# Optimization experiments

Hardware: AMD Instinct MI355X
Metric: run time of the kernel (lower is better)

Reference implementation:

```python
import jax, jax.numpy as jnp
import numpy as np

CAPACITY_FACTOR = 1.25  # config.capacity_factor


def setup_inputs() -> dict:
    key = jax.random.key(0)
    ks = jax.random.split(key, 5)
    B, S, D, F, E = 8, 2048, 768, 3072, 8
    return {
        "x": jax.random.normal(ks[0], (B, S, D), jnp.float32),
        "switch_w": jax.random.normal(ks[1], (D, E), jnp.float32) * 0.02,
        "switch_b": jnp.zeros((E,), jnp.float32),
        "w1": jax.random.normal(ks[2], (E, D, F), jnp.float32) * 0.02,
        "b1": jnp.zeros((E, F), jnp.float32),
        "w2": jax.random.normal(ks[3], (E, F, D), jnp.float32) * 0.02,
        "b2": jnp.zeros((E, D), jnp.float32),
    }


def reference(x, switch_w, switch_b, w1, b1, w2, b2):
    B, S, D = x.shape
    E = w1.shape[0]
    xf = x.reshape(-1, D)                      # [N, D] tokens
    N = xf.shape[0]
    capacity = int(CAPACITY_FACTOR * N / E)

    # top-1 switch routing
    probs = jax.nn.softmax(xf @ switch_w + switch_b, axis=-1)   # [N, E]
    prob_max = jnp.max(probs, axis=-1)                          # [N]
    routes = jnp.argmax(probs, axis=-1)                         # [N] int

    # priority drop: within each expert keep the `capacity` tokens with
    # highest gate prob. Rank tokens within their expert by descending prob.
    sort_idx = jnp.lexsort((-prob_max, routes))                 # [N]
    counts = jnp.bincount(routes, length=E)
    starts = jnp.concatenate([jnp.zeros((1,), counts.dtype), jnp.cumsum(counts)[:-1]])
    rank_sorted = jnp.arange(N) - starts[routes[sort_idx]]
    rank = jnp.zeros((N,), jnp.int32).at[sort_idx].set(rank_sorted.astype(jnp.int32))
    keep = rank < capacity

    # dispatch kept tokens into [E, capacity, D]; overflow goes to slot E
    dest_e = jnp.where(keep, routes, E)
    dest_c = jnp.where(keep, rank, 0)
    buf = jnp.zeros((E + 1, capacity, D), xf.dtype).at[dest_e, dest_c].set(xf)

    # per-expert FFN (grouped GEMM), GELU is exact (erf) as in nn.GELU()
    h = jax.nn.gelu(jnp.einsum('ecd,edf->ecf', buf[:E], w1) + b1[:, None, :],
                    approximate=False)
    o = jnp.einsum('ecf,efd->ecd', h, w2) + b2[:, None, :]      # [E, cap, D]

    # combine: kept tokens get expert output, dropped tokens pass through x
    y_exp = o[routes, dest_c]                                    # [N, D]
    y = jnp.where(keep[:, None], y_exp, xf)
    out = y * prob_max[:, None]                                  # is_scale_prob
    return out.reshape(B, S, D)
```

## Files before the change

kernel.cpp:

```cpp
#include <hip/hip_runtime.h>
#include <cstdint>
#include <cstddef>

#define E_ 8
#define D_ 768
#define F_ 3072
#define N_ 16384
#define CAP_ 2560
#define NCHUNK_ (N_ / 256)

typedef __attribute__((ext_vector_type(8))) short bf16x8;
typedef __attribute__((ext_vector_type(4))) float f32x4;

__device__ __forceinline__ unsigned short f2bf(float f) {
  unsigned u = __float_as_uint(f);
  u += 0x7fffu + ((u >> 16) & 1u);
  return (unsigned short)(u >> 16);
}

__device__ __forceinline__ void gload16(const void* g, void* l) {
  __builtin_amdgcn_global_load_lds(
      (const __attribute__((address_space(1))) void*)g,
      (__attribute__((address_space(3))) void*)l, 16, 0, 0);
}

__global__ void tcast_kernel(const float* __restrict__ src, unsigned short* __restrict__ dst,
                             int R, int C) {
  __shared__ float tile[64][65];
  int e = blockIdx.z;
  const float* s = src + (size_t)e * R * C;
  unsigned short* d = dst + (size_t)e * R * C;
  int c0 = blockIdx.x * 64, r0 = blockIdx.y * 64;
  int tx = threadIdx.x, ty = threadIdx.y;
  #pragma unroll
  for (int rr = ty; rr < 64; rr += 8) {
    tile[rr][tx]      = s[(size_t)(r0 + rr) * C + c0 + tx];
    tile[rr][tx + 32] = s[(size_t)(r0 + rr) * C + c0 + tx + 32];
  }
  __syncthreads();
  #pragma unroll
  for (int cc = ty; cc < 64; cc += 8) {
    ushort2 o;
    o.x = f2bf(tile[2 * tx][cc]);
    o.y = f2bf(tile[2 * tx + 1][cc]);
    *(ushort2*)&d[(size_t)(c0 + cc) * R + r0 + 2 * tx] = o;
  }
}

__global__ __launch_bounds__(256) void router_kernel(
    const float* __restrict__ x, const float* __restrict__ sw, const float* __restrict__ sb,
    int* __restrict__ route, float* __restrict__ prob,
    unsigned short* __restrict__ xb) {
  __shared__ float wl[E_ * D_];
  int tid = threadIdx.x;
  #pragma unroll
  for (int ee = 0; ee < E_; ++ee)
    for (int dd = tid; dd < D_; dd += 256)
      wl[ee * D_ + dd] = sw[dd * E_ + ee];
  __syncthreads();
  int wave = tid >> 6, lane = tid & 63;
  int tbase = blockIdx.x * 16 + wave * 4;
  #pragma unroll
  for (int tt = 0; tt < 4; ++tt) {
    int t = tbase + tt;
    const float* xp = x + (size_t)t * D_;
    unsigned short* xbp = xb + (size_t)t * D_;
    float acc[E_];
    #pragma unroll
    for (int e = 0; e < E_; ++e) acc[e] = 0.f;
    #pragma unroll
    for (int r = 0; r < D_ / 64; ++r) {
      int dd = r * 64 + lane;
      float xv = xp[dd];
      xbp[dd] = f2bf(xv);
      #pragma unroll
      for (int e = 0; e < E_; ++e) acc[e] += xv * wl[e * D_ + dd];
    }
    #pragma unroll
    for (int e = 0; e < E_; ++e) {
      #pragma unroll
      for (int o = 32; o > 0; o >>= 1) acc[e] += __shfl_xor(acc[e], o);
    }
    if (lane == 0) {
      float mx = -1e30f; int arg = 0;
      #pragma unroll
      for (int e = 0; e < E_; ++e) {
        float l = acc[e] + sb[e];
        acc[e] = l;
        if (l > mx) { mx = l; arg = e; }
      }
      float s = 0.f;
      #pragma unroll
      for (int e = 0; e < E_; ++e) s += expf(acc[e] - mx);
      route[t] = arg;
      prob[t] = 1.f / s;
    }
  }
}

__global__ void hist_kernel(const int* __restrict__ route, int* __restrict__ chunk_hist) {
  __shared__ int h[E_];
  int tid = threadIdx.x;
  if (tid < E_) h[tid] = 0;
  __syncthreads();
  atomicAdd(&h[route[blockIdx.x * 256 + tid]], 1);
  __syncthreads();
  if (tid < E_) chunk_hist[blockIdx.x * E_ + tid] = h[tid];
}

__global__ void scan_kernel(const int* __restrict__ chunk_hist, int* __restrict__ chunk_off,
                            int* __restrict__ counts) {
  __shared__ int h[NCHUNK_ * E_];
  int tid = threadIdx.x;
  h[tid] = chunk_hist[tid];
  __syncthreads();
  if (tid < E_) {
    int run = 0;
    for (int c = 0; c < NCHUNK_; ++c) {
      chunk_off[c * E_ + tid] = run;
      run += h[c * E_ + tid];
    }
    counts[tid] = run;
  }
}

__global__ void assign_kernel(const int* __restrict__ route, const float* __restrict__ prob,
                              const int* __restrict__ counts, const int* __restrict__ chunk_off,
                              int* __restrict__ tok_list, int* __restrict__ slot) {
  __shared__ int rt[256];
  int tid = threadIdx.x;
  int i = blockIdx.x * 256 + tid;
  int e = route[i];
  rt[tid] = e;
  __syncthreads();
  int r = 0;
  for (int j = 0; j < tid; ++j) r += (rt[j] == e) ? 1 : 0;
  int c = counts[e];
  int s; bool keep;
  if (c <= CAP_) {
    s = chunk_off[blockIdx.x * E_ + e] + r;
    keep = true;
  } else {
    float p = prob[i];
    int rr = 0;
    for (int j = 0; j < N_; ++j) {
      if (route[j] == e) {
        float pj = prob[j];
        rr += (pj > p || (pj == p && j < i)) ? 1 : 0;
      }
    }
    s = rr; keep = (rr < CAP_);
  }
  if (keep) tok_list[e * CAP_ + s] = i;
  slot[i] = keep ? s : -1;
}

__global__ __launch_bounds__(256) void gemm1_kernel(
    const unsigned short* __restrict__ xb, const unsigned short* __restrict__ w1t,
    const float* __restrict__ b1, const int* __restrict__ tok_list,
    const int* __restrict__ counts, unsigned short* __restrict__ hb) {
  int e = blockIdx.z;
  int Me = counts[e] < CAP_ ? counts[e] : CAP_;
  int m0 = blockIdx.x * 128;
  if (m0 >= Me) return;
  int n0 = blockIdx.y * 128;
  __shared__ unsigned short At[128 * 32];
  __shared__ unsigned short Bt[128 * 32];
  int tid = threadIdx.x, lane = tid & 63, wave = tid >> 6;
  int rA0 = (wave * 2 + 0) * 16 + (lane >> 2);
  int rA1 = (wave * 2 + 1) * 16 + (lane >> 2);
  int cb = (lane & 3) * 16;
  int mr0 = m0 + rA0; if (mr0 > Me - 1) mr0 = Me - 1;
  int mr1 = m0 + rA1; if (mr1 > Me - 1) mr1 = Me - 1;
  int tok0 = tok_list[e * CAP_ + mr0];
  int tok1 = tok_list[e * CAP_ + mr1];
  const char* gA0 = (const char*)(xb + (size_t)tok0 * D_) + cb;
  const char* gA1 = (const char*)(xb + (size_t)tok1 * D_) + cb;
  const char* gB0 = (const char*)(w1t + ((size_t)e * F_ + n0 + rA0) * D_) + cb;
  const char* gB1 = (const char*)(w1t + ((size_t)e * F_ + n0 + rA1) * D_) + cb;
  unsigned short* lA0 = At + (wave * 2 + 0) * 512;
  unsigned short* lA1 = At + (wave * 2 + 1) * 512;
  unsigned short* lB0 = Bt + (wave * 2 + 0) * 512;
  unsigned short* lB1 = Bt + (wave * 2 + 1) * 512;
  f32x4 acc[4][4] = {};
  int wm = (wave >> 1) * 64, wn = (wave & 1) * 64;
  int fr = lane & 15, fk = (lane >> 4) * 8;
  for (int k0 = 0; k0 < D_; k0 += 32) {
    __syncthreads();
    gload16(gA0 + (size_t)2 * k0, lA0);
    gload16(gA1 + (size_t)2 * k0, lA1);
    gload16(gB0 + (size_t)2 * k0, lB0);
    gload16(gB1 + (size_t)2 * k0, lB1);
    __syncthreads();
    bf16x8 a[4], b[4];
    #pragma unroll
    for (int i = 0; i < 4; ++i)
      a[i] = *(const bf16x8*)(At + (wm + i * 16 + fr) * 32 + fk);
    #pragma unroll
    for (int j = 0; j < 4; ++j)
      b[j] = *(const bf16x8*)(Bt + (wn + j * 16 + fr) * 32 + fk);
    #pragma unroll
    for (int i = 0; i < 4; ++i)
      #pragma unroll
      for (int j = 0; j < 4; ++j)
        acc[i][j] = __builtin_amdgcn_mfma_f32_16x16x32_bf16(a[i], b[j], acc[i][j], 0, 0, 0);
  }
  int q4 = (lane >> 4) * 4;
  #pragma unroll
  for (int i = 0; i < 4; ++i) {
    #pragma unroll
    for (int j = 0; j < 4; ++j) {
      int col = n0 + wn + j * 16 + (lane & 15);
      float bias = b1[e * F_ + col];
      #pragma unroll
      for (int r = 0; r < 4; ++r) {
        int row = m0 + wm + i * 16 + q4 + r;
        if (row < Me) {
          float v = acc[i][j][r] + bias;
          v = 0.5f * v * (1.f + erff(v * 0.70710678118654752f));
          hb[((size_t)e * CAP_ + row) * F_ + col] = f2bf(v);
        }
      }
    }
  }
}

__global__ __launch_bounds__(256) void gemm2_kernel(
    const unsigned short* __restrict__ hb, const unsigned short* __restrict__ w2t,
    const float* __restrict__ b2, const int* __restrict__ tok_list,
    const int* __restrict__ counts, const float* __restrict__ prob,
    float* __restrict__ out) {
  int e = blockIdx.z;
  int Me = counts[e] < CAP_ ? counts[e] : CAP_;
  int m0 = blockIdx.x * 128;
  if (m0 >= Me) return;
  int n0 = blockIdx.y * 128;
  __shared__ unsigned short At[128 * 32];
  __shared__ unsigned short Bt[128 * 32];
  int tid = threadIdx.x, lane = tid & 63, wave = tid >> 6;
  int rA0 = (wave * 2 + 0) * 16 + (lane >> 2);
  int rA1 = (wave * 2 + 1) * 16 + (lane >> 2);
  int cb = (lane & 3) * 16;
  const char* gA0 = (const char*)(hb + ((size_t)e * CAP_ + m0 + rA0) * F_) + cb;
  const char* gA1 = (const char*)(hb + ((size_t)e * CAP_ + m0 + rA1) * F_) + cb;
  const char* gB0 = (const char*)(w2t + ((size_t)e * D_ + n0 + rA0) * F_) + cb;
  const char* gB1 = (const char*)(w2t + ((size_t)e * D_ + n0 + rA1) * F_) + cb;
  unsigned short* lA0 = At + (wave * 2 + 0) * 512;
  unsigned short* lA1 = At + (wave * 2 + 1) * 512;
  unsigned short* lB0 = Bt + (wave * 2 + 0) * 512;
  unsigned short* lB1 = Bt + (wave * 2 + 1) * 512;
  f32x4 acc[4][4] = {};
  int wm = (wave >> 1) * 64, wn = (wave & 1) * 64;
  int fr = lane & 15, fk = (lane >> 4) * 8;
  for (int k0 = 0; k0 < F_; k0 += 32) {
    __syncthreads();
    gload16(gA0 + (size_t)2 * k0, lA0);
    gload16(gA1 + (size_t)2 * k0, lA1);
    gload16(gB0 + (size_t)2 * k0, lB0);
    gload16(gB1 + (size_t)2 * k0, lB1);
    __syncthreads();
    bf16x8 a[4], b[4];
    #pragma unroll
    for (int i = 0; i < 4; ++i)
      a[i] = *(const bf16x8*)(At + (wm + i * 16 + fr) * 32 + fk);
    #pragma unroll
    for (int j = 0; j < 4; ++j)
      b[j] = *(const bf16x8*)(Bt + (wn + j * 16 + fr) * 32 + fk);
    #pragma unroll
    for (int i = 0; i < 4; ++i)
      #pragma unroll
      for (int j = 0; j < 4; ++j)
        acc[i][j] = __builtin_amdgcn_mfma_f32_16x16x32_bf16(a[i], b[j], acc[i][j], 0, 0, 0);
  }
  int q4 = (lane >> 4) * 4;
  #pragma unroll
  for (int i = 0; i < 4; ++i) {
    #pragma unroll
    for (int r = 0; r < 4; ++r) {
      int row = m0 + wm + i * 16 + q4 + r;
      if (row < Me) {
        int tok = tok_list[e * CAP_ + row];
        float pm = prob[tok];
        #pragma unroll
        for (int j = 0; j < 4; ++j) {
          int col = n0 + wn + j * 16 + (lane & 15);
          float v = (acc[i][j][r] + b2[e * D_ + col]) * pm;
          out[(size_t)tok * D_ + col] = v;
        }
      }
    }
  }
}

__global__ void passthrough_kernel(const float* __restrict__ x, const float* __restrict__ prob,
                                   const int* __restrict__ slot, float* __restrict__ out) {
  int t = blockIdx.x;
  if (slot[t] >= 0) return;
  float p = prob[t];
  for (int d = threadIdx.x; d < D_; d += 256)
    out[(size_t)t * D_ + d] = x[(size_t)t * D_ + d] * p;
}

extern "C" void kernel_launch(void* const* d_in, const int* in_sizes, int n_in,
                              void* d_out, int out_size, void* d_ws, size_t ws_size,
                              hipStream_t stream) {
  const float* x  = (const float*)d_in[0];
  const float* sw = (const float*)d_in[1];
  const float* sb = (const float*)d_in[2];
  const float* w1 = (const float*)d_in[3];
  const float* b1 = (const float*)d_in[4];
  const float* w2 = (const float*)d_in[5];
  const float* b2 = (const float*)d_in[6];
  float* out = (float*)d_out;
  (void)in_sizes; (void)n_in; (void)out_size; (void)ws_size;

  char* ws = (char*)d_ws;
  size_t off = 0;
  auto alloc = [&](size_t bytes) {
    char* p = ws + off;
    off = (off + bytes + 255) & ~(size_t)255;
    return p;
  };
  int* counts     = (int*)alloc(32 * sizeof(int));
  int* chunk_hist = (int*)alloc((size_t)NCHUNK_ * E_ * sizeof(int));
  int* chunk_off  = (int*)alloc((size_t)NCHUNK_ * E_ * sizeof(int));
  int* tok_list   = (int*)alloc((size_t)E_ * CAP_ * sizeof(int));
  int* route      = (int*)alloc((size_t)N_ * 4);
  float* prob     = (float*)alloc((size_t)N_ * 4);
  int* slot       = (int*)alloc((size_t)N_ * 4);
  unsigned short* xb  = (unsigned short*)alloc((size_t)N_ * D_ * 2);
  unsigned short* w1t = (unsigned short*)alloc((size_t)E_ * D_ * F_ * 2);
  unsigned short* w2t = (unsigned short*)alloc((size_t)E_ * D_ * F_ * 2);
  unsigned short* hb  = (unsigned short*)alloc((size_t)E_ * CAP_ * F_ * 2);

  dim3 tb(32, 8);
  tcast_kernel<<<dim3(F_ / 64, D_ / 64, E_), tb, 0, stream>>>(w1, w1t, D_, F_);
  tcast_kernel<<<dim3(D_ / 64, F_ / 64, E_), tb, 0, stream>>>(w2, w2t, F_, D_);
  router_kernel<<<N_ / 16, 256, 0, stream>>>(x, sw, sb, route, prob, xb);
  hist_kernel<<<NCHUNK_, 256, 0, stream>>>(route, chunk_hist);
  scan_kernel<<<1, NCHUNK_ * E_, 0, stream>>>(chunk_hist, chunk_off, counts);
  assign_kernel<<<NCHUNK_, 256, 0, stream>>>(route, prob, counts, chunk_off, tok_list, slot);
  gemm1_kernel<<<dim3(CAP_ / 128, F_ / 128, E_), 256, 0, stream>>>(xb, w1t, b1, tok_list, counts, hb);
  gemm2_kernel<<<dim3(CAP_ / 128, D_ / 128, E_), 256, 0, stream>>>(hb, w2t, b2, tok_list, counts, prob, out);
  passthrough_kernel<<<N_, 256, 0, stream>>>(x, prob, slot, out);
}
```

Before: 590.4 us.

## Use 256x256 double-buffered swizzled LDS tiles in expert GEMMs

Both expert GEMMs move from 128x128 tiles with a K=32 single-buffer loop to 256x256 tiles with K=64, 512 threads and a 128KB double-buffered LDS ring. The next K-tile loads overlap the MFMAs on the current one, and an XOR swizzle is meant to avoid LDS bank conflicts; s_setprio is raised around the MFMA sequence. The aim is more operand reuse per loaded byte and fewer barriers. In exchange, registers per thread roughly double and gemm2 launches only 3 N-tiles per expert, so the grid gets small and may underfill the GPU.

```diff
diff --git a/kernel.cpp b/kernel.cpp
--- a/kernel.cpp
+++ b/kernel.cpp
@@ -155,62 +155,86 @@
   slot[i] = keep ? s : -1;
 }
 
-__global__ __launch_bounds__(256) void gemm1_kernel(
+
+__global__ __launch_bounds__(512, 2) void gemm1_kernel(
     const unsigned short* __restrict__ xb, const unsigned short* __restrict__ w1t,
     const float* __restrict__ b1, const int* __restrict__ tok_list,
     const int* __restrict__ counts, unsigned short* __restrict__ hb) {
   int e = blockIdx.z;
   int Me = counts[e] < CAP_ ? counts[e] : CAP_;
-  int m0 = blockIdx.x * 128;
+  int m0 = blockIdx.x * 256;
   if (m0 >= Me) return;
-  int n0 = blockIdx.y * 128;
-  __shared__ unsigned short At[128 * 32];
-  __shared__ unsigned short Bt[128 * 32];
-  int tid = threadIdx.x, lane = tid & 63, wave = tid >> 6;
-  int rA0 = (wave * 2 + 0) * 16 + (lane >> 2);
-  int rA1 = (wave * 2 + 1) * 16 + (lane >> 2);
-  int cb = (lane & 3) * 16;
-  int mr0 = m0 + rA0; if (mr0 > Me - 1) mr0 = Me - 1;
-  int mr1 = m0 + rA1; if (mr1 > Me - 1) mr1 = Me - 1;
-  int tok0 = tok_list[e * CAP_ + mr0];
-  int tok1 = tok_list[e * CAP_ + mr1];
-  const char* gA0 = (const char*)(xb + (size_t)tok0 * D_) + cb;
-  const char* gA1 = (const char*)(xb + (size_t)tok1 * D_) + cb;
-  const char* gB0 = (const char*)(w1t + ((size_t)e * F_ + n0 + rA0) * D_) + cb;
-  const char* gB1 = (const char*)(w1t + ((size_t)e * F_ + n0 + rA1) * D_) + cb;
-  unsigned short* lA0 = At + (wave * 2 + 0) * 512;
-  unsigned short* lA1 = At + (wave * 2 + 1) * 512;
-  unsigned short* lB0 = Bt + (wave * 2 + 0) * 512;
-  unsigned short* lB1 = Bt + (wave * 2 + 1) * 512;
-  f32x4 acc[4][4] = {};
-  int wm = (wave >> 1) * 64, wn = (wave & 1) * 64;
-  int fr = lane & 15, fk = (lane >> 4) * 8;
-  for (int k0 = 0; k0 < D_; k0 += 32) {
+  int n0 = blockIdx.y * 256;
+  __shared__ unsigned short sm[65536];
+  int tid = threadIdx.x, lane = tid & 63, w = tid >> 6;
+  int srow = w * 8 + (lane >> 3);
+  int schunk = (lane & 7) ^ (lane >> 3);
+  unsigned dstA = (unsigned)(w * 512);
+  const char* sA[4];
+  #pragma unroll
+  for (int ar = 0; ar < 4; ++ar) {
+    int rw = m0 + ar * 64 + srow;
+    if (rw > Me - 1) rw = Me - 1;
+    int tok = tok_list[e * CAP_ + rw];
+    sA[ar] = (const char*)(xb + (size_t)tok * D_) + schunk * 16;
+  }
+  const char* sB = (const char*)(w1t + ((size_t)e * F_ + n0 + srow) * D_) + schunk * 16;
+  const size_t BR = (size_t)64 * D_ * 2;
+  int fr = lane & 15, q = lane >> 4;
+  int wm = (w >> 2) * 128, wn = (w & 3) * 64;
+  f32x4 acc[8][4] = {};
+
+  #pragma unroll
+  for (int ar = 0; ar < 4; ++ar) {
+    gload16(sA[ar], sm + ar * 4096 + dstA);
+    gload16(sB + ar * BR, sm + 16384 + ar * 4096 + dstA);
+  }
+  __syncthreads();
+
+  const int NT = D_ / 64;
+  for (int kt = 0; kt < NT; ++kt) {
+    int cb = kt & 1;
+    if (kt + 1 < NT) {
+      int ob = cb ^ 1;
+      size_t ko = (size_t)(kt + 1) * 128;
+      #pragma unroll
+      for (int ar = 0; ar < 4; ++ar) {
+        gload16(sA[ar] + ko, sm + ob * 32768 + ar * 4096 + dstA);
+        gload16(sB + ar * BR + ko, sm + ob * 32768 + 16384 + ar * 4096 + dstA);
+      }
+    }
+    const unsigned short* A  = sm + cb * 32768;
+    const unsigned short* Bm = A + 16384;
+    #pragma unroll
+    for (int kh = 0; kh < 2; ++kh) {
+      bf16x8 bfr[4];
+      #pragma unroll
+      for (int j = 0; j < 4; ++j) {
+        int row = wn + j * 16 + fr;
+        int pc = (kh * 4 + q) ^ (fr & 7);
+        bfr[j] = *(const bf16x8*)(Bm + row * 64 + pc * 8);
+      }
+      __builtin_amdgcn_s_setprio(1);
+      #pragma unroll
+      for (int i = 0; i < 8; ++i) {
+        int row = wm + i * 16 + fr;
+        int pc = (kh * 4 + q) ^ (fr & 7);
+        bf16x8 afr = *(const bf16x8*)(A + row * 64 + pc * 8);
+        #pragma unroll
+        for (int j = 0; j < 4; ++j)
+          acc[i][j] = __builtin_amdgcn_mfma_f32_16x16x32_bf16(afr, bfr[j], acc[i][j], 0, 0, 0);
+      }
+      __builtin_amdgcn_s_setprio(0);
+    }
     __syncthreads();
-    gload16(gA0 + (size_t)2 * k0, lA0);
-    gload16(gA1 + (size_t)2 * k0, lA1);
-    gload16(gB0 + (size_t)2 * k0, lB0);
-    gload16(gB1 + (size_t)2 * k0, lB1);
-    __syncthreads();
-    bf16x8 a[4], b[4];
-    #pragma unroll
-    for (int i = 0; i < 4; ++i)
-      a[i] = *(const bf16x8*)(At + (wm + i * 16 + fr) * 32 + fk);
-    #pragma unroll
-    for (int j = 0; j < 4; ++j)
-      b[j] = *(const bf16x8*)(Bt + (wn + j * 16 + fr) * 32 + fk);
-    #pragma unroll
-    for (int i = 0; i < 4; ++i)
-      #pragma unroll
-      for (int j = 0; j < 4; ++j)
-        acc[i][j] = __builtin_amdgcn_mfma_f32_16x16x32_bf16(a[i], b[j], acc[i][j], 0, 0, 0);
-  }
-  int q4 = (lane >> 4) * 4;
-  #pragma unroll
-  for (int i = 0; i < 4; ++i) {
+  }
+
+  int q4 = q * 4;
+  #pragma unroll
+  for (int i = 0; i < 8; ++i) {
     #pragma unroll
     for (int j = 0; j < 4; ++j) {
-      int col = n0 + wn + j * 16 + (lane & 15);
+      int col = n0 + wn + j * 16 + fr;
       float bias = b1[e * F_ + col];
       #pragma unroll
       for (int r = 0; r < 4; ++r) {
@@ -225,56 +249,79 @@
   }
 }
 
-__global__ __launch_bounds__(256) void gemm2_kernel(
+__global__ __launch_bounds__(512, 2) void gemm2_kernel(
     const unsigned short* __restrict__ hb, const unsigned short* __restrict__ w2t,
     const float* __restrict__ b2, const int* __restrict__ tok_list,
     const int* __restrict__ counts, const float* __restrict__ prob,
     float* __restrict__ out) {
   int e = blockIdx.z;
   int Me = counts[e] < CAP_ ? counts[e] : CAP_;
-  int m0 = blockIdx.x * 128;
+  int m0 = blockIdx.x * 256;
   if (m0 >= Me) return;
-  int n0 = blockIdx.y * 128;
-  __shared__ unsigned short At[128 * 32];
-  __shared__ unsigned short Bt[128 * 32];
-  int tid = threadIdx.x, lane = tid & 63, wave = tid >> 6;
-  int rA0 = (wave * 2 + 0) * 16 + (lane >> 2);
-  int rA1 = (wave * 2 + 1) * 16 + (lane >> 2);
-  int cb = (lane & 3) * 16;
-  const char* gA0 = (const char*)(hb + ((size_t)e * CAP_ + m0 + rA0) * F_) + cb;
-  const char* gA1 = (const char*)(hb + ((size_t)e * CAP_ + m0 + rA1) * F_) + cb;
-  const char* gB0 = (const char*)(w2t + ((size_t)e * D_ + n0 + rA0) * F_) + cb;
-  const char* gB1 = (const char*)(w2t + ((size_t)e * D_ + n0 + rA1) * F_) + cb;
-  unsigned short* lA0 = At + (wave * 2 + 0) * 512;
-  unsigned short* lA1 = At + (wave * 2 + 1) * 512;
-  unsigned short* lB0 = Bt + (wave * 2 + 0) * 512;
-  unsigned short* lB1 = Bt + (wave * 2 + 1) * 512;
-  f32x4 acc[4][4] = {};
-  int wm = (wave >> 1) * 64, wn = (wave & 1) * 64;
-  int fr = lane & 15, fk = (lane >> 4) * 8;
-  for (int k0 = 0; k0 < F_; k0 += 32) {
+  int n0 = blockIdx.y * 256;
+  __shared__ unsigned short sm[65536];
+  int tid = threadIdx.x, lane = tid & 63, w = tid >> 6;
+  int srow = w * 8 + (lane >> 3);
+  int schunk = (lane & 7) ^ (lane >> 3);
+  unsigned dstA = (unsigned)(w * 512);
+  const char* sA[4];
+  #pragma unroll
+  for (int ar = 0; ar < 4; ++ar)
+    sA[ar] = (const char*)(hb + ((size_t)e * CAP_ + m0 + ar * 64 + srow) * F_) + schunk * 16;
+  const char* sB = (const char*)(w2t + ((size_t)e * D_ + n0 + srow) * F_) + schunk * 16;
+  const size_t BR = (size_t)64 * F_ * 2;
+  int fr = lane & 15, q = lane >> 4;
+  int wm = (w >> 2) * 128, wn = (w & 3) * 64;
+  f32x4 acc[8][4] = {};
+
+  #pragma unroll
+  for (int ar = 0; ar < 4; ++ar) {
+    gload16(sA[ar], sm + ar * 4096 + dstA);
+    gload16(sB + ar * BR, sm + 16384 + ar * 4096 + dstA);
+  }
+  __syncthreads();
+
+  const int NT = F_ / 64;
+  for (int kt = 0; kt < NT; ++kt) {
+    int cb = kt & 1;
+    if (kt + 1 < NT) {
+      int ob = cb ^ 1;
+      size_t ko = (size_t)(kt + 1) * 128;
+      #pragma unroll
+      for (int ar = 0; ar < 4; ++ar) {
+        gload16(sA[ar] + ko, sm + ob * 32768 + ar * 4096 + dstA);
+        gload16(sB + ar * BR + ko, sm + ob * 32768 + 16384 + ar * 4096 + dstA);
+      }
+    }
+    const unsigned short* A  = sm + cb * 32768;
+    const unsigned short* Bm = A + 16384;
+    #pragma unroll
+    for (int kh = 0; kh < 2; ++kh) {
+      bf16x8 bfr[4];
+      #pragma unroll
+      for (int j = 0; j < 4; ++j) {
+        int row = wn + j * 16 + fr;
+        int pc = (kh * 4 + q) ^ (fr & 7);
+        bfr[j] = *(const bf16x8*)(Bm + row * 64 + pc * 8);
+      }
+      __builtin_amdgcn_s_setprio(1);
+      #pragma unroll
+      for (int i = 0; i < 8; ++i) {
+        int row = wm + i * 16 + fr;
+        int pc = (kh * 4 + q) ^ (fr & 7);
+        bf16x8 afr = *(const bf16x8*)(A + row * 64 + pc * 8);
+        #pragma unroll
+        for (int j = 0; j < 4; ++j)
+          acc[i][j] = __builtin_amdgcn_mfma_f32_16x16x32_bf16(afr, bfr[j], acc[i][j], 0, 0, 0);
+      }
+      __builtin_amdgcn_s_setprio(0);
+    }
     __syncthreads();
-    gload16(gA0 + (size_t)2 * k0, lA0);
-    gload16(gA1 + (size_t)2 * k0, lA1);
-    gload16(gB0 + (size_t)2 * k0, lB0);
-    gload16(gB1 + (size_t)2 * k0, lB1);
-    __syncthreads();
-    bf16x8 a[4], b[4];
-    #pragma unroll
-    for (int i = 0; i < 4; ++i)
-      a[i] = *(const bf16x8*)(At + (wm + i * 16 + fr) * 32 + fk);
-    #pragma unroll
-    for (int j = 0; j < 4; ++j)
-      b[j] = *(const bf16x8*)(Bt + (wn + j * 16 + fr) * 32 + fk);
-    #pragma unroll
-    for (int i = 0; i < 4; ++i)
-      #pragma unroll
-      for (int j = 0; j < 4; ++j)
-        acc[i][j] = __builtin_amdgcn_mfma_f32_16x16x32_bf16(a[i], b[j], acc[i][j], 0, 0, 0);
-  }
-  int q4 = (lane >> 4) * 4;
-  #pragma unroll
-  for (int i = 0; i < 4; ++i) {
+  }
+
+  int q4 = q * 4;
+  #pragma unroll
+  for (int i = 0; i < 8; ++i) {
     #pragma unroll
     for (int r = 0; r < 4; ++r) {
       int row = m0 + wm + i * 16 + q4 + r;
@@ -283,7 +330,7 @@
         float pm = prob[tok];
         #pragma unroll
         for (int j = 0; j < 4; ++j) {
-          int col = n0 + wn + j * 16 + (lane & 15);
+          int col = n0 + wn + j * 16 + fr;
           float v = (acc[i][j][r] + b2[e * D_ + col]) * pm;
           out[(size_t)tok * D_ + col] = v;
         }
@@ -340,7 +387,7 @@
   hist_kernel<<<NCHUNK_, 256, 0, stream>>>(route, chunk_hist);
   scan_kernel<<<1, NCHUNK_ * E_, 0, stream>>>(chunk_hist, chunk_off, counts);
   assign_kernel<<<NCHUNK_, 256, 0, stream>>>(route, prob, counts, chunk_off, tok_list, slot);
-  gemm1_kernel<<<dim3(CAP_ / 128, F_ / 128, E_), 256, 0, stream>>>(xb, w1t, b1, tok_list, counts, hb);
-  gemm2_kernel<<<dim3(CAP_ / 128, D_ / 128, E_), 256, 0, stream>>>(hb, w2t, b2, tok_list, counts, prob, out);
+  gemm1_kernel<<<dim3(CAP_ / 256, F_ / 256, E_), 512, 0, stream>>>(xb, w1t, b1, tok_list, counts, hb);
+  gemm2_kernel<<<dim3(CAP_ / 256, D_ / 256, E_), 512, 0, stream>>>(hb, w2t, b2, tok_list, counts, prob, out);
   passthrough_kernel<<<N_, 256, 0, stream>>>(x, prob, slot, out);
 }
```

Result: faster. 554.1 us (-6.1%).

## Rewrite expert GEMMs with 256x256 tiles, double-buffered LDS pipeline, swizzle and XCD remap

Applied to the files above, without the earlier changes.

Both grouped GEMM kernels move from 128x128 tiles with a single LDS buffer and two barriers per K step to 256x256 tiles with 512 threads. The new loop double-buffers 64-wide K tiles in LDS, stores them with an XOR swizzle, and interleaves async global-to-LDS loads with MFMA groups using explicit barriers, s_setprio and vmcnt waits. A block-index remap spreads work across the XCDs for better L2 locality. The aim is to hide load latency, cut LDS bank conflicts and raise arithmetic intensity, at the cost of 128KB of LDS and more registers per block, more idle work on partial tiles, and fewer blocks for gemm2.

```diff
diff --git a/kernel.cpp b/kernel.cpp
--- a/kernel.cpp
+++ b/kernel.cpp
@@ -155,62 +155,108 @@
   slot[i] = keep ? s : -1;
 }
 
-__global__ __launch_bounds__(256) void gemm1_kernel(
+
+#define RD_A(dst, cb, i0)                                                         \
+  _Pragma("unroll") for (int ii = 0; ii < 4; ++ii)                                \
+  _Pragma("unroll") for (int kh = 0; kh < 2; ++kh)                                \
+    dst[ii][kh] = *(const bf16x8*)(sm + (cb) * 32768 + wmo +                      \
+        ((i0 + ii) * 16 + fr) * 64 + (((kh * 4 + q) ^ fr7) * 8));
+
+#define RD_B(dst, cb, j0)                                                         \
+  _Pragma("unroll") for (int jj = 0; jj < 2; ++jj)                                \
+  _Pragma("unroll") for (int kh = 0; kh < 2; ++kh)                                \
+    dst[jj][kh] = *(const bf16x8*)(sm + (cb) * 32768 + 16384 + wno +              \
+        (wn64 + (j0 + jj) * 16 + fr) * 64 + (((kh * 4 + q) ^ fr7) * 8));
+
+#define MM(i0, j0, A_, B_)                                                        \
+  _Pragma("unroll") for (int ii = 0; ii < 4; ++ii)                                \
+  _Pragma("unroll") for (int jj = 0; jj < 2; ++jj)                                \
+  _Pragma("unroll") for (int kh = 0; kh < 2; ++kh)                                \
+    acc[i0 + ii][j0 + jj] = __builtin_amdgcn_mfma_f32_16x16x32_bf16(              \
+        A_[ii][kh], B_[jj][kh], acc[i0 + ii][j0 + jj], 0, 0, 0);
+
+#define STG_A(tb, h, t) {                                                         \
+  gload16(pA##h##0 + (size_t)(t) * 64, smb + (tb) * 65536 + (h) * 16384 + w * 1024);            \
+  gload16(pA##h##1 + (size_t)(t) * 64, smb + (tb) * 65536 + (h) * 16384 + 8192 + w * 1024); }
+
+#define STG_B(tb, h, t) {                                                         \
+  gload16(pB##h##0 + (size_t)(t) * 64, smb + (tb) * 65536 + 32768 + (h) * 16384 + w * 1024);    \
+  gload16(pB##h##1 + (size_t)(t) * 64, smb + (tb) * 65536 + 32768 + (h) * 16384 + 8192 + w * 1024); }
+
+#define BAR __builtin_amdgcn_s_barrier()
+#define PRIO1 __builtin_amdgcn_s_setprio(1)
+#define PRIO0 __builtin_amdgcn_s_setprio(0)
+#define WAITV4 asm volatile("s_waitcnt vmcnt(4)" ::: "memory")
+
+#define GROUP(cb, ta, tgtA, tb_, tgtB)                                            \
+  RD_A(alo, cb, 0); RD_B(blo, cb, 0); STG_A(tgtA, 0, ta);                         \
+  BAR; PRIO1; MM(0, 0, alo, blo); PRIO0; BAR;                                     \
+  RD_B(bhi, cb, 2); STG_A(tgtA, 1, ta);                                           \
+  BAR; PRIO1; MM(0, 2, alo, bhi); PRIO0; BAR;                                     \
+  RD_A(ahi, cb, 4); STG_B(tgtB, 0, tb_);                                          \
+  BAR; PRIO1; MM(4, 0, ahi, blo); PRIO0; BAR;                                     \
+  STG_B(tgtB, 1, tb_);                                                            \
+  BAR; PRIO1; MM(4, 2, ahi, bhi); PRIO0; WAITV4; BAR;
+
+__global__ __launch_bounds__(512, 2) void gemm1_kernel(
     const unsigned short* __restrict__ xb, const unsigned short* __restrict__ w1t,
     const float* __restrict__ b1, const int* __restrict__ tok_list,
     const int* __restrict__ counts, unsigned short* __restrict__ hb) {
-  int e = blockIdx.z;
+  int flat = blockIdx.x + 10 * (blockIdx.y + 12 * blockIdx.z);
+  int work = (flat & 7) * 120 + (flat >> 3);
+  int xm = work % 10;
+  int rest = work / 10;
+  int yn = rest % 12;
+  int e = rest / 12;
   int Me = counts[e] < CAP_ ? counts[e] : CAP_;
-  int m0 = blockIdx.x * 128;
+  int m0 = xm * 256;
   if (m0 >= Me) return;
-  int n0 = blockIdx.y * 128;
-  __shared__ unsigned short At[128 * 32];
-  __shared__ unsigned short Bt[128 * 32];
-  int tid = threadIdx.x, lane = tid & 63, wave = tid >> 6;
-  int rA0 = (wave * 2 + 0) * 16 + (lane >> 2);
-  int rA1 = (wave * 2 + 1) * 16 + (lane >> 2);
-  int cb = (lane & 3) * 16;
-  int mr0 = m0 + rA0; if (mr0 > Me - 1) mr0 = Me - 1;
-  int mr1 = m0 + rA1; if (mr1 > Me - 1) mr1 = Me - 1;
-  int tok0 = tok_list[e * CAP_ + mr0];
-  int tok1 = tok_list[e * CAP_ + mr1];
-  const char* gA0 = (const char*)(xb + (size_t)tok0 * D_) + cb;
-  const char* gA1 = (const char*)(xb + (size_t)tok1 * D_) + cb;
-  const char* gB0 = (const char*)(w1t + ((size_t)e * F_ + n0 + rA0) * D_) + cb;
-  const char* gB1 = (const char*)(w1t + ((size_t)e * F_ + n0 + rA1) * D_) + cb;
-  unsigned short* lA0 = At + (wave * 2 + 0) * 512;
-  unsigned short* lA1 = At + (wave * 2 + 1) * 512;
-  unsigned short* lB0 = Bt + (wave * 2 + 0) * 512;
-  unsigned short* lB1 = Bt + (wave * 2 + 1) * 512;
-  f32x4 acc[4][4] = {};
-  int wm = (wave >> 1) * 64, wn = (wave & 1) * 64;
-  int fr = lane & 15, fk = (lane >> 4) * 8;
-  for (int k0 = 0; k0 < D_; k0 += 32) {
-    __syncthreads();
-    gload16(gA0 + (size_t)2 * k0, lA0);
-    gload16(gA1 + (size_t)2 * k0, lA1);
-    gload16(gB0 + (size_t)2 * k0, lB0);
-    gload16(gB1 + (size_t)2 * k0, lB1);
-    __syncthreads();
-    bf16x8 a[4], b[4];
-    #pragma unroll
-    for (int i = 0; i < 4; ++i)
-      a[i] = *(const bf16x8*)(At + (wm + i * 16 + fr) * 32 + fk);
-    #pragma unroll
-    for (int j = 0; j < 4; ++j)
-      b[j] = *(const bf16x8*)(Bt + (wn + j * 16 + fr) * 32 + fk);
-    #pragma unroll
-    for (int i = 0; i < 4; ++i)
-      #pragma unroll
-      for (int j = 0; j < 4; ++j)
-        acc[i][j] = __builtin_amdgcn_mfma_f32_16x16x32_bf16(a[i], b[j], acc[i][j], 0, 0, 0);
-  }
-  int q4 = (lane >> 4) * 4;
-  #pragma unroll
-  for (int i = 0; i < 4; ++i) {
+  int n0 = yn * 256;
+  __shared__ unsigned short sm[65536];
+  char* smb = (char*)sm;
+  int tid = threadIdx.x, lane = tid & 63, w = tid >> 6;
+  int l8 = lane >> 3;
+  int sc = (lane & 7) ^ l8;
+  int rbase = w * 8 + l8;
+  int ra00 = m0 + rbase;       if (ra00 > Me - 1) ra00 = Me - 1;
+  int ra01 = m0 + 64 + rbase;  if (ra01 > Me - 1) ra01 = Me - 1;
+  int ra10 = m0 + 128 + rbase; if (ra10 > Me - 1) ra10 = Me - 1;
+  int ra11 = m0 + 192 + rbase; if (ra11 > Me - 1) ra11 = Me - 1;
+  const unsigned short* pA00 = xb + (size_t)tok_list[e * CAP_ + ra00] * D_ + sc * 8;
+  const unsigned short* pA01 = xb + (size_t)tok_list[e * CAP_ + ra01] * D_ + sc * 8;
+  const unsigned short* pA10 = xb + (size_t)tok_list[e * CAP_ + ra10] * D_ + sc * 8;
+  const unsigned short* pA11 = xb + (size_t)tok_list[e * CAP_ + ra11] * D_ + sc * 8;
+  const unsigned short* pB00 = w1t + ((size_t)e * F_ + n0 + rbase) * D_ + sc * 8;
+  const unsigned short* pB01 = w1t + ((size_t)e * F_ + n0 + 64 + rbase) * D_ + sc * 8;
+  const unsigned short* pB10 = w1t + ((size_t)e * F_ + n0 + 128 + rbase) * D_ + sc * 8;
+  const unsigned short* pB11 = w1t + ((size_t)e * F_ + n0 + 192 + rbase) * D_ + sc * 8;
+  int fr = lane & 15, q = lane >> 4, fr7 = fr & 7;
+  int wm = (w >> 2) * 128, wn = (w & 3) * 64;
+  int wmo = wm * 64;
+  int wno = (wn & 128) * 64;
+  int wn64 = wn & 64;
+  f32x4 acc[8][4] = {};
+  bf16x8 alo[4][2], ahi[4][2], blo[2][2], bhi[2][2];
+
+  STG_B(0, 0, 0); STG_B(0, 1, 0); STG_A(0, 0, 0); STG_A(0, 1, 0);
+  STG_B(1, 0, 1); STG_B(1, 1, 1);
+  WAITV4; BAR;
+
+  const int NT = D_ / 64;
+  for (int it = 0; it < NT / 2; ++it) {
+    int t1 = 2 * it + 1, t2 = 2 * it + 2, t3 = 2 * it + 3;
+    if (t2 > NT - 1) t2 = NT - 1;
+    if (t3 > NT - 1) t3 = NT - 1;
+    GROUP(0, t1, 1, t2, 0)
+    GROUP(1, t2, 0, t3, 1)
+  }
+
+  int q4 = q * 4;
+  #pragma unroll
+  for (int i = 0; i < 8; ++i) {
     #pragma unroll
     for (int j = 0; j < 4; ++j) {
-      int col = n0 + wn + j * 16 + (lane & 15);
+      int col = n0 + wn + j * 16 + fr;
       float bias = b1[e * F_ + col];
       #pragma unroll
       for (int r = 0; r < 4; ++r) {
@@ -225,56 +271,59 @@
   }
 }
 
-__global__ __launch_bounds__(256) void gemm2_kernel(
+__global__ __launch_bounds__(512, 2) void gemm2_kernel(
     const unsigned short* __restrict__ hb, const unsigned short* __restrict__ w2t,
     const float* __restrict__ b2, const int* __restrict__ tok_list,
     const int* __restrict__ counts, const float* __restrict__ prob,
     float* __restrict__ out) {
-  int e = blockIdx.z;
+  int flat = blockIdx.x + 10 * (blockIdx.y + 3 * blockIdx.z);
+  int work = (flat & 7) * 30 + (flat >> 3);
+  int xm = work % 10;
+  int rest = work / 10;
+  int yn = rest % 3;
+  int e = rest / 3;
   int Me = counts[e] < CAP_ ? counts[e] : CAP_;
-  int m0 = blockIdx.x * 128;
+  int m0 = xm * 256;
   if (m0 >= Me) return;
-  int n0 = blockIdx.y * 128;
-  __shared__ unsigned short At[128 * 32];
-  __shared__ unsigned short Bt[128 * 32];
-  int tid = threadIdx.x, lane = tid & 63, wave = tid >> 6;
-  int rA0 = (wave * 2 + 0) * 16 + (lane >> 2);
-  int rA1 = (wave * 2 + 1) * 16 + (lane >> 2);
-  int cb = (lane & 3) * 16;
-  const char* gA0 = (const char*)(hb + ((size_t)e * CAP_ + m0 + rA0) * F_) + cb;
-  const char* gA1 = (const char*)(hb + ((size_t)e * CAP_ + m0 + rA1) * F_) + cb;
-  const char* gB0 = (const char*)(w2t + ((size_t)e * D_ + n0 + rA0) * F_) + cb;
-  const char* gB1 = (const char*)(w2t + ((size_t)e * D_ + n0 + rA1) * F_) + cb;
-  unsigned short* lA0 = At + (wave * 2 + 0) * 512;
-  unsigned short* lA1 = At + (wave * 2 + 1) * 512;
-  unsigned short* lB0 = Bt + (wave * 2 + 0) * 512;
-  unsigned short* lB1 = Bt + (wave * 2 + 1) * 512;
-  f32x4 acc[4][4] = {};
-  int wm = (wave >> 1) * 64, wn = (wave & 1) * 64;
-  int fr = lane & 15, fk = (lane >> 4) * 8;
-  for (int k0 = 0; k0 < F_; k0 += 32) {
-    __syncthreads();
-    gload16(gA0 + (size_t)2 * k0, lA0);
-    gload16(gA1 + (size_t)2 * k0, lA1);
-    gload16(gB0 + (size_t)2 * k0, lB0);
-    gload16(gB1 + (size_t)2 * k0, lB1);
-    __syncthreads();
-    bf16x8 a[4], b[4];
-    #pragma unroll
-    for (int i = 0; i < 4; ++i)
-      a[i] = *(const bf16x8*)(At + (wm + i * 16 + fr) * 32 + fk);
-    #pragma unroll
-    for (int j = 0; j < 4; ++j)
-      b[j] = *(const bf16x8*)(Bt + (wn + j * 16 + fr) * 32 + fk);
-    #pragma unroll
-    for (int i = 0; i < 4; ++i)
-      #pragma unroll
-      for (int j = 0; j < 4; ++j)
-        acc[i][j] = __builtin_amdgcn_mfma_f32_16x16x32_bf16(a[i], b[j], acc[i][j], 0, 0, 0);
-  }
-  int q4 = (lane >> 4) * 4;
-  #pragma unroll
-  for (int i = 0; i < 4; ++i) {
+  int n0 = yn * 256;
+  __shared__ unsigned short sm[65536];
+  char* smb = (char*)sm;
+  int tid = threadIdx.x, lane = tid & 63, w = tid >> 6;
+  int l8 = lane >> 3;
+  int sc = (lane & 7) ^ l8;
+  int rbase = w * 8 + l8;
+  const unsigned short* pA00 = hb + ((size_t)e * CAP_ + m0 + rbase) * F_ + sc * 8;
+  const unsigned short* pA01 = hb + ((size_t)e * CAP_ + m0 + 64 + rbase) * F_ + sc * 8;
+  const unsigned short* pA10 = hb + ((size_t)e * CAP_ + m0 + 128 + rbase) * F_ + sc * 8;
+  const unsigned short* pA11 = hb + ((size_t)e * CAP_ + m0 + 192 + rbase) * F_ + sc * 8;
+  const unsigned short* pB00 = w2t + ((size_t)e * D_ + n0 + rbase) * F_ + sc * 8;
+  const unsigned short* pB01 = w2t + ((size_t)e * D_ + n0 + 64 + rbase) * F_ + sc * 8;
+  const unsigned short* pB10 = w2t + ((size_t)e * D_ + n0 + 128 + rbase) * F_ + sc * 8;
+  const unsigned short* pB11 = w2t + ((size_t)e * D_ + n0 + 192 + rbase) * F_ + sc * 8;
+  int fr = lane & 15, q = lane >> 4, fr7 = fr & 7;
+  int wm = (w >> 2) * 128, wn = (w & 3) * 64;
+  int wmo = wm * 64;
+  int wno = (wn & 128) * 64;
+  int wn64 = wn & 64;
+  f32x4 acc[8][4] = {};
+  bf16x8 alo[4][2], ahi[4][2], blo[2][2], bhi[2][2];
+
+  STG_B(0, 0, 0); STG_B(0, 1, 0); STG_A(0, 0, 0); STG_A(0, 1, 0);
+  STG_B(1, 0, 1); STG_B(1, 1, 1);
+  WAITV4; BAR;
+
+  const int NT = F_ / 64;
+  for (int it = 0; it < NT / 2; ++it) {
+    int t1 = 2 * it + 1, t2 = 2 * it + 2, t3 = 2 * it + 3;
+    if (t2 > NT - 1) t2 = NT - 1;
+    if (t3 > NT - 1) t3 = NT - 1;
+    GROUP(0, t1, 1, t2, 0)
+    GROUP(1, t2, 0, t3, 1)
+  }
+
+  int q4 = q * 4;
+  #pragma unroll
+  for (int i = 0; i < 8; ++i) {
     #pragma unroll
     for (int r = 0; r < 4; ++r) {
       int row = m0 + wm + i * 16 + q4 + r;
@@ -283,7 +332,7 @@
         float pm = prob[tok];
         #pragma unroll
         for (int j = 0; j < 4; ++j) {
-          int col = n0 + wn + j * 16 + (lane & 15);
+          int col = n0 + wn + j * 16 + fr;
           float v = (acc[i][j][r] + b2[e * D_ + col]) * pm;
           out[(size_t)tok * D_ + col] = v;
         }
@@ -340,7 +389,7 @@
   hist_kernel<<<NCHUNK_, 256, 0, stream>>>(route, chunk_hist);
   scan_kernel<<<1, NCHUNK_ * E_, 0, stream>>>(chunk_hist, chunk_off, counts);
   assign_kernel<<<NCHUNK_, 256, 0, stream>>>(route, prob, counts, chunk_off, tok_list, slot);
-  gemm1_kernel<<<dim3(CAP_ / 128, F_ / 128, E_), 256, 0, stream>>>(xb, w1t, b1, tok_list, counts, hb);
-  gemm2_kernel<<<dim3(CAP_ / 128, D_ / 128, E_), 256, 0, stream>>>(hb, w2t, b2, tok_list, counts, prob, out);
+  gemm1_kernel<<<dim3(10, 12, 8), 512, 0, stream>>>(xb, w1t, b1, tok_list, counts, hb);
+  gemm2_kernel<<<dim3(10, 3, 8), 512, 0, stream>>>(hb, w2t, b2, tok_list, counts, prob, out);
   passthrough_kernel<<<N_, 256, 0, stream>>>(x, prob, slot, out);
 }
```

Result: slower. 624.9 us (+5.8%).

## Deepen GEMM K-tile to 64 with XOR-swizzled LDS and XCD-aware block remap

Applied to the files above, without the earlier changes.

Both expert GEMMs now stage a 128x64 K-slice per iteration (double the previous depth) with an XOR swizzle on the LDS layout to avoid bank conflicts. This halves the number of barrier pairs per output tile. Blocks are remapped so that consecutive hardware-dispatched blocks land on the same expert across XCDs, aiming to improve L2 reuse of weights. The weight transpose-cast kernel also writes 8-byte vectors instead of 4-byte ones. LDS usage per block doubles to 32KB, which may reduce occupancy.

```diff
diff --git a/kernel.cpp b/kernel.cpp
--- a/kernel.cpp
+++ b/kernel.cpp
@@ -38,12 +38,17 @@
     tile[rr][tx + 32] = s[(size_t)(r0 + rr) * C + c0 + tx + 32];
   }
   __syncthreads();
-  #pragma unroll
-  for (int cc = ty; cc < 64; cc += 8) {
-    ushort2 o;
-    o.x = f2bf(tile[2 * tx][cc]);
-    o.y = f2bf(tile[2 * tx + 1][cc]);
-    *(ushort2*)&d[(size_t)(c0 + cc) * R + r0 + 2 * tx] = o;
+  int rr = 4 * (tx & 15);
+  int ccb = (tx >> 4) + 2 * ty;
+  #pragma unroll
+  for (int m = 0; m < 4; ++m) {
+    int cc = ccb + 16 * m;
+    ushort4 o;
+    o.x = f2bf(tile[rr + 0][cc]);
+    o.y = f2bf(tile[rr + 1][cc]);
+    o.z = f2bf(tile[rr + 2][cc]);
+    o.w = f2bf(tile[rr + 3][cc]);
+    *(ushort4*)&d[(size_t)(c0 + cc) * R + r0 + rr] = o;
   }
 }
 
@@ -155,62 +160,81 @@
   slot[i] = keep ? s : -1;
 }
 
+
+#define STAGE8(ko)                                            \
+  gload16(pA0 + (ko), smw + 0 * 4096 + w * 1024);             \
+  gload16(pA1 + (ko), smw + 1 * 4096 + w * 1024);             \
+  gload16(pA2 + (ko), smw + 2 * 4096 + w * 1024);             \
+  gload16(pA3 + (ko), smw + 3 * 4096 + w * 1024);             \
+  gload16(pB0 + (ko), smw + 16384 + 0 * 4096 + w * 1024);     \
+  gload16(pB1 + (ko), smw + 16384 + 1 * 4096 + w * 1024);     \
+  gload16(pB2 + (ko), smw + 16384 + 2 * 4096 + w * 1024);     \
+  gload16(pB3 + (ko), smw + 16384 + 3 * 4096 + w * 1024);
+
+#define MFMA16(A_, B_)                                                            \
+  _Pragma("unroll") for (int i = 0; i < 4; ++i)                                   \
+  _Pragma("unroll") for (int j = 0; j < 4; ++j)                                   \
+    acc[i][j] = __builtin_amdgcn_mfma_f32_16x16x32_bf16(A_[i], B_[j], acc[i][j], 0, 0, 0);
+
 __global__ __launch_bounds__(256) void gemm1_kernel(
     const unsigned short* __restrict__ xb, const unsigned short* __restrict__ w1t,
     const float* __restrict__ b1, const int* __restrict__ tok_list,
     const int* __restrict__ counts, unsigned short* __restrict__ hb) {
-  int e = blockIdx.z;
+  int flat = blockIdx.x + 20 * (blockIdx.y + 24 * blockIdx.z);
+  int work = (flat & 7) * 480 + (flat >> 3);
+  int e = work / 480;
+  int rem = work % 480;
+  int xm = rem % 20, yn = rem / 20;
   int Me = counts[e] < CAP_ ? counts[e] : CAP_;
-  int m0 = blockIdx.x * 128;
+  int m0 = xm * 128;
   if (m0 >= Me) return;
-  int n0 = blockIdx.y * 128;
-  __shared__ unsigned short At[128 * 32];
-  __shared__ unsigned short Bt[128 * 32];
-  int tid = threadIdx.x, lane = tid & 63, wave = tid >> 6;
-  int rA0 = (wave * 2 + 0) * 16 + (lane >> 2);
-  int rA1 = (wave * 2 + 1) * 16 + (lane >> 2);
-  int cb = (lane & 3) * 16;
-  int mr0 = m0 + rA0; if (mr0 > Me - 1) mr0 = Me - 1;
-  int mr1 = m0 + rA1; if (mr1 > Me - 1) mr1 = Me - 1;
-  int tok0 = tok_list[e * CAP_ + mr0];
-  int tok1 = tok_list[e * CAP_ + mr1];
-  const char* gA0 = (const char*)(xb + (size_t)tok0 * D_) + cb;
-  const char* gA1 = (const char*)(xb + (size_t)tok1 * D_) + cb;
-  const char* gB0 = (const char*)(w1t + ((size_t)e * F_ + n0 + rA0) * D_) + cb;
-  const char* gB1 = (const char*)(w1t + ((size_t)e * F_ + n0 + rA1) * D_) + cb;
-  unsigned short* lA0 = At + (wave * 2 + 0) * 512;
-  unsigned short* lA1 = At + (wave * 2 + 1) * 512;
-  unsigned short* lB0 = Bt + (wave * 2 + 0) * 512;
-  unsigned short* lB1 = Bt + (wave * 2 + 1) * 512;
+  int n0 = yn * 128;
+  __shared__ unsigned short sm[16384];
+  char* smw = (char*)sm;
+  const char* smc = (const char*)sm;
+  int tid = threadIdx.x, lane = tid & 63, w = tid >> 6;
+  int l8 = lane >> 3;
+  int sc = (lane & 7) ^ l8;
+  int rbase = w * 8 + l8;
+  int r0_ = m0 + rbase;       if (r0_ > Me - 1) r0_ = Me - 1;
+  int r1_ = m0 + 32 + rbase;  if (r1_ > Me - 1) r1_ = Me - 1;
+  int r2_ = m0 + 64 + rbase;  if (r2_ > Me - 1) r2_ = Me - 1;
+  int r3_ = m0 + 96 + rbase;  if (r3_ > Me - 1) r3_ = Me - 1;
+  const unsigned short* pA0 = xb + (size_t)tok_list[e * CAP_ + r0_] * D_ + sc * 8;
+  const unsigned short* pA1 = xb + (size_t)tok_list[e * CAP_ + r1_] * D_ + sc * 8;
+  const unsigned short* pA2 = xb + (size_t)tok_list[e * CAP_ + r2_] * D_ + sc * 8;
+  const unsigned short* pA3 = xb + (size_t)tok_list[e * CAP_ + r3_] * D_ + sc * 8;
+  const unsigned short* pB0 = w1t + ((size_t)e * F_ + n0 + rbase) * D_ + sc * 8;
+  const unsigned short* pB1 = w1t + ((size_t)e * F_ + n0 + 32 + rbase) * D_ + sc * 8;
+  const unsigned short* pB2 = w1t + ((size_t)e * F_ + n0 + 64 + rbase) * D_ + sc * 8;
+  const unsigned short* pB3 = w1t + ((size_t)e * F_ + n0 + 96 + rbase) * D_ + sc * 8;
+  int fr = lane & 15, q = lane >> 4, fr7 = fr & 7;
+  int wm = (w >> 1) * 64, wn = (w & 1) * 64;
+  unsigned aoff = (unsigned)((wm + fr) * 128 + ((q ^ fr7) * 16));
+  unsigned boff = (unsigned)(16384 + (wn + fr) * 128 + ((q ^ fr7) * 16));
   f32x4 acc[4][4] = {};
-  int wm = (wave >> 1) * 64, wn = (wave & 1) * 64;
-  int fr = lane & 15, fk = (lane >> 4) * 8;
-  for (int k0 = 0; k0 < D_; k0 += 32) {
+  for (int k0 = 0; k0 < D_; k0 += 64) {
     __syncthreads();
-    gload16(gA0 + (size_t)2 * k0, lA0);
-    gload16(gA1 + (size_t)2 * k0, lA1);
-    gload16(gB0 + (size_t)2 * k0, lB0);
-    gload16(gB1 + (size_t)2 * k0, lB1);
+    STAGE8((size_t)k0)
     __syncthreads();
     bf16x8 a[4], b[4];
     #pragma unroll
-    for (int i = 0; i < 4; ++i)
-      a[i] = *(const bf16x8*)(At + (wm + i * 16 + fr) * 32 + fk);
-    #pragma unroll
-    for (int j = 0; j < 4; ++j)
-      b[j] = *(const bf16x8*)(Bt + (wn + j * 16 + fr) * 32 + fk);
-    #pragma unroll
-    for (int i = 0; i < 4; ++i)
-      #pragma unroll
-      for (int j = 0; j < 4; ++j)
-        acc[i][j] = __builtin_amdgcn_mfma_f32_16x16x32_bf16(a[i], b[j], acc[i][j], 0, 0, 0);
-  }
-  int q4 = (lane >> 4) * 4;
+    for (int i = 0; i < 4; ++i) a[i] = *(const bf16x8*)(smc + aoff + i * 2048);
+    #pragma unroll
+    for (int j = 0; j < 4; ++j) b[j] = *(const bf16x8*)(smc + boff + j * 2048);
+    MFMA16(a, b)
+    #pragma unroll
+    for (int i = 0; i < 4; ++i) a[i] = *(const bf16x8*)(smc + (aoff ^ 64u) + i * 2048);
+    #pragma unroll
+    for (int j = 0; j < 4; ++j) b[j] = *(const bf16x8*)(smc + (boff ^ 64u) + j * 2048);
+    MFMA16(a, b)
+  }
+  int q4 = q * 4;
   #pragma unroll
   for (int i = 0; i < 4; ++i) {
     #pragma unroll
     for (int j = 0; j < 4; ++j) {
-      int col = n0 + wn + j * 16 + (lane & 15);
+      int col = n0 + wn + j * 16 + fr;
       float bias = b1[e * F_ + col];
       #pragma unroll
       for (int r = 0; r < 4; ++r) {
@@ -230,49 +254,52 @@
     const float* __restrict__ b2, const int* __restrict__ tok_list,
     const int* __restrict__ counts, const float* __restrict__ prob,
     float* __restrict__ out) {
-  int e = blockIdx.z;
+  int flat = blockIdx.x + 20 * (blockIdx.y + 6 * blockIdx.z);
+  int work = (flat & 7) * 120 + (flat >> 3);
+  int e = work / 120;
+  int rem = work % 120;
+  int xm = rem % 20, yn = rem / 20;
   int Me = counts[e] < CAP_ ? counts[e] : CAP_;
-  int m0 = blockIdx.x * 128;
+  int m0 = xm * 128;
   if (m0 >= Me) return;
-  int n0 = blockIdx.y * 128;
-  __shared__ unsigned short At[128 * 32];
-  __shared__ unsigned short Bt[128 * 32];
-  int tid = threadIdx.x, lane = tid & 63, wave = tid >> 6;
-  int rA0 = (wave * 2 + 0) * 16 + (lane >> 2);
-  int rA1 = (wave * 2 + 1) * 16 + (lane >> 2);
-  int cb = (lane & 3) * 16;
-  const char* gA0 = (const char*)(hb + ((size_t)e * CAP_ + m0 + rA0) * F_) + cb;
-  const char* gA1 = (const char*)(hb + ((size_t)e * CAP_ + m0 + rA1) * F_) + cb;
-  const char* gB0 = (const char*)(w2t + ((size_t)e * D_ + n0 + rA0) * F_) + cb;
-  const char* gB1 = (const char*)(w2t + ((size_t)e * D_ + n0 + rA1) * F_) + cb;
-  unsigned short* lA0 = At + (wave * 2 + 0) * 512;
-  unsigned short* lA1 = At + (wave * 2 + 1) * 512;
-  unsigned short* lB0 = Bt + (wave * 2 + 0) * 512;
-  unsigned short* lB1 = Bt + (wave * 2 + 1) * 512;
+  int n0 = yn * 128;
+  __shared__ unsigned short sm[16384];
+  char* smw = (char*)sm;
+  const char* smc = (const char*)sm;
+  int tid = threadIdx.x, lane = tid & 63, w = tid >> 6;
+  int l8 = lane >> 3;
+  int sc = (lane & 7) ^ l8;
+  int rbase = w * 8 + l8;
+  const unsigned short* pA0 = hb + ((size_t)e * CAP_ + m0 + rbase) * F_ + sc * 8;
+  const unsigned short* pA1 = hb + ((size_t)e * CAP_ + m0 + 32 + rbase) * F_ + sc * 8;
+  const unsigned short* pA2 = hb + ((size_t)e * CAP_ + m0 + 64 + rbase) * F_ + sc * 8;
+  const unsigned short* pA3 = hb + ((size_t)e * CAP_ + m0 + 96 + rbase) * F_ + sc * 8;
+  const unsigned short* pB0 = w2t + ((size_t)e * D_ + n0 + rbase) * F_ + sc * 8;
+  const unsigned short* pB1 = w2t + ((size_t)e * D_ + n0 + 32 + rbase) * F_ + sc * 8;
+  const unsigned short* pB2 = w2t + ((size_t)e * D_ + n0 + 64 + rbase) * F_ + sc * 8;
+  const unsigned short* pB3 = w2t + ((size_t)e * D_ + n0 + 96 + rbase) * F_ + sc * 8;
+  int fr = lane & 15, q = lane >> 4, fr7 = fr & 7;
+  int wm = (w >> 1) * 64, wn = (w & 1) * 64;
+  unsigned aoff = (unsigned)((wm + fr) * 128 + ((q ^ fr7) * 16));
+  unsigned boff = (unsigned)(16384 + (wn + fr) * 128 + ((q ^ fr7) * 16));
   f32x4 acc[4][4] = {};
-  int wm = (wave >> 1) * 64, wn = (wave & 1) * 64;
-  int fr = lane & 15, fk = (lane >> 4) * 8;
-  for (int k0 = 0; k0 < F_; k0 += 32) {
+  for (int k0 = 0; k0 < F_; k0 += 64) {
     __syncthreads();
-    gload16(gA0 + (size_t)2 * k0, lA0);
-    gload16(gA1 + (size_t)2 * k0, lA1);
-    gload16(gB0 + (size_t)2 * k0, lB0);
-    gload16(gB1 + (size_t)2 * k0, lB1);
+    STAGE8((size_t)k0)
     __syncthreads();
     bf16x8 a[4], b[4];
     #pragma unroll
-    for (int i = 0; i < 4; ++i)
-      a[i] = *(const bf16x8*)(At + (wm + i * 16 + fr) * 32 + fk);
-    #pragma unroll
-    for (int j = 0; j < 4; ++j)
-      b[j] = *(const bf16x8*)(Bt + (wn + j * 16 + fr) * 32 + fk);
-    #pragma unroll
-    for (int i = 0; i < 4; ++i)
-      #pragma unroll
-      for (int j = 0; j < 4; ++j)
-        acc[i][j] = __builtin_amdgcn_mfma_f32_16x16x32_bf16(a[i], b[j], acc[i][j], 0, 0, 0);
-  }
-  int q4 = (lane >> 4) * 4;
+    for (int i = 0; i < 4; ++i) a[i] = *(const bf16x8*)(smc + aoff + i * 2048);
+    #pragma unroll
+    for (int j = 0; j < 4; ++j) b[j] = *(const bf16x8*)(smc + boff + j * 2048);
+    MFMA16(a, b)
+    #pragma unroll
+    for (int i = 0; i < 4; ++i) a[i] = *(const bf16x8*)(smc + (aoff ^ 64u) + i * 2048);
+    #pragma unroll
+    for (int j = 0; j < 4; ++j) b[j] = *(const bf16x8*)(smc + (boff ^ 64u) + j * 2048);
+    MFMA16(a, b)
+  }
+  int q4 = q * 4;
   #pragma unroll
   for (int i = 0; i < 4; ++i) {
     #pragma unroll
@@ -283,7 +310,7 @@
         float pm = prob[tok];
         #pragma unroll
         for (int j = 0; j < 4; ++j) {
-          int col = n0 + wn + j * 16 + (lane & 15);
+          int col = n0 + wn + j * 16 + fr;
           float v = (acc[i][j][r] + b2[e * D_ + col]) * pm;
           out[(size_t)tok * D_ + col] = v;
         }
@@ -340,7 +367,7 @@
   hist_kernel<<<NCHUNK_, 256, 0, stream>>>(route, chunk_hist);
   scan_kernel<<<1, NCHUNK_ * E_, 0, stream>>>(chunk_hist, chunk_off, counts);
   assign_kernel<<<NCHUNK_, 256, 0, stream>>>(route, prob, counts, chunk_off, tok_list, slot);
-  gemm1_kernel<<<dim3(CAP_ / 128, F_ / 128, E_), 256, 0, stream>>>(xb, w1t, b1, tok_list, counts, hb);
-  gemm2_kernel<<<dim3(CAP_ / 128, D_ / 128, E_), 256, 0, stream>>>(hb, w2t, b2, tok_list, counts, prob, out);
+  gemm1_kernel<<<dim3(20, 24, 8), 256, 0, stream>>>(xb, w1t, b1, tok_list, counts, hb);
+  gemm2_kernel<<<dim3(20, 6, 8), 256, 0, stream>>>(hb, w2t, b2, tok_list, counts, prob, out);
   passthrough_kernel<<<N_, 256, 0, stream>>>(x, prob, slot, out);
 }
```

Result: slower. 625.1 us (+5.9%).
